# Optimization experiments

Hardware: AMD Instinct MI355X
Metric: run time of the kernel (lower is better)

The kernel has to match this reference:

```python
import math
import jax, jax.numpy as jnp
import numpy as np

NUM_HEADS = 16


def setup_inputs() -> dict:
    key = jax.random.key(0)
    ks = jax.random.split(key, 5)
    B, S, H = 2, 2048, 1024
    hidden_states = jax.random.normal(ks[0], (B, S, H), dtype=jnp.float32)
    # causal lower-triangular float mask [1, 1, S, S], as the module expects
    ltor_mask = jnp.tril(jnp.ones((S, S), dtype=jnp.float32))[None, None, :, :]
    # weights stored pre-transposed: y = x @ W + b (equivalent to torch Linear)
    W_qkv = jax.random.normal(ks[1], (H, 3 * H), dtype=jnp.float32) * (1.0 / math.sqrt(H))
    b_qkv = jnp.zeros((3 * H,), dtype=jnp.float32)
    W_dense = jax.random.normal(ks[2], (H, H), dtype=jnp.float32) * (1.0 / math.sqrt(H))
    b_dense = jnp.zeros((H,), dtype=jnp.float32)
    return {
        "hidden_states": hidden_states,
        "ltor_mask": ltor_mask,
        "W_qkv": W_qkv,
        "b_qkv": b_qkv,
        "W_dense": W_dense,
        "b_dense": b_dense,
    }


def reference(hidden_states, ltor_mask, W_qkv, b_qkv, W_dense, b_dense):
    B, S, H = hidden_states.shape
    nh = NUM_HEADS
    hd = H // nh

    # fused QKV projection: [B, S, 3H] -> split -> [B, nh, S, hd]
    qkv = hidden_states @ W_qkv + b_qkv
    q, k, v = jnp.split(qkv, 3, axis=-1)

    def to_heads(x):
        return x.reshape(B, S, nh, hd).transpose(0, 2, 1, 3)

    q, k, v = to_heads(q), to_heads(k), to_heads(v)

    # scaled dot-product scores [B, nh, S, S]
    scores = jnp.einsum("bhqd,bhkd->bhqk", q, k) / math.sqrt(hd)
    # mul/sub causal masking, exactly as the torch module does
    scores = scores * ltor_mask - 10000.0 * (1.0 - ltor_mask)
    probs = jax.nn.softmax(scores, axis=-1)
    # attention dropout omitted (eval mode / p=0.0)

    ctx = jnp.einsum("bhqk,bhkd->bhqd", probs, v)
    ctx = ctx.transpose(0, 2, 1, 3).reshape(B, S, H)

    out = ctx @ W_dense + b_dense
    # output dropout omitted (eval mode / p=0.0)
    return out
```

## Files before the change

kernel.cpp:

```cpp
#include <hip/hip_runtime.h>
#include <math.h>

#define BATCH 2
#define SEQ   2048
#define HID   1024
#define NHEAD 16
#define HDIM  64
#define MTOT  (BATCH * SEQ)
#define QKVN  (3 * HID)
#define HBUF  ((size_t)BATCH * NHEAD * SEQ * HDIM)

typedef _Float16 f16x8 __attribute__((ext_vector_type(8)));
typedef _Float16 f16x4 __attribute__((ext_vector_type(4)));
typedef float    f32x4 __attribute__((ext_vector_type(4)));

#define MFMA16(a, b, c) __builtin_amdgcn_mfma_f32_16x16x32_f16((a), (b), (c), 0, 0, 0)

#define GLDS16(gp, lp) __builtin_amdgcn_global_load_lds( \
    (const __attribute__((address_space(1))) void*)(gp), \
    (__attribute__((address_space(3))) void*)(lp), 16, 0, 0)

#if __has_builtin(__builtin_amdgcn_exp2f)
#define EXP2F(x) __builtin_amdgcn_exp2f(x)
#else
#define EXP2F(x) exp2f(x)
#endif

#define SCALE2 0.18033688011f
#define MASK2  -14426.950408f
#define BIAS2  -4.0f

__global__ __launch_bounds__(256) void prep_kernel(
    const float* __restrict__ hs, const float* __restrict__ Wqkv,
    const float* __restrict__ Wd, _Float16* __restrict__ A_h,
    _Float16* __restrict__ outQ, _Float16* __restrict__ outD)
{
    __shared__ _Float16 T[32][36];
    const int gid = blockIdx.x;
    const int tid = threadIdx.x;
    if (gid < 2048) {
        const int ci = gid * 256 + tid;
        const int m = ci >> 7, cc = ci & 127;
        const int g = cc >> 2, c = cc & 3;
        const float* src = hs + (size_t)m * 1024 + cc * 8;
        f16x8 o;
#pragma unroll
        for (int j = 0; j < 8; ++j) o[j] = (_Float16)src[j];
        *(f16x8*)(A_h + (size_t)m * 1024 + g * 32 + ((c ^ (m & 3)) << 3)) = o;
        return;
    }
    const int tb = gid - 2048;
    const int bx = tb & 127, k0 = (tb >> 7) * 32;
    const float* in;
    _Float16* out;
    int N, n0;
    if (bx < 96) { in = Wqkv; out = outQ; N = QKVN; n0 = bx * 32; }
    else         { in = Wd;   out = outD; N = HID;  n0 = (bx - 96) * 32; }
    {
        const int r = tid >> 3, c4 = (tid & 7) * 4;
        float4 v = *(const float4*)(in + (size_t)(k0 + r) * N + n0 + c4);
        T[r][c4 + 0] = (_Float16)v.x;
        T[r][c4 + 1] = (_Float16)v.y;
        T[r][c4 + 2] = (_Float16)v.z;
        T[r][c4 + 3] = (_Float16)v.w;
    }
    __syncthreads();
    {
        const int nn = tid >> 3, k4 = (tid & 7) * 4;
        const int n = n0 + nn;
        f16x4 o;
        o[0] = T[k4 + 0][nn]; o[1] = T[k4 + 1][nn];
        o[2] = T[k4 + 2][nn]; o[3] = T[k4 + 3][nn];
        const int pos = ((k4 >> 3) ^ (n & 3)), half = (k4 >> 2) & 1;
        *(f16x4*)(out + (size_t)n * 1024 + k0 + pos * 8 + half * 4) = o;
    }
}

__global__ __launch_bounds__(256) void transpose_v(
    const _Float16* __restrict__ v, _Float16* __restrict__ vt)
{
    __shared__ _Float16 T[64 * 64];
    const int s0 = blockIdx.x * 64;
    const size_t bh = (size_t)blockIdx.z * NHEAD + blockIdx.y;
    const int tid = threadIdx.x;
#pragma unroll
    for (int pass = 0; pass < 2; ++pass) {
        const int s = pass * 32 + (tid >> 3);
        const int c = tid & 7;
        f16x8 val = *(const f16x8*)(v + (bh * SEQ + s0 + s) * 64 + c * 8);
#pragma unroll
        for (int j = 0; j < 8; ++j) {
            const int d = c * 8 + j;
            T[d * 64 + (((s >> 3) ^ (d & 7)) << 3) + (s & 7)] = val[j];
        }
    }
    __syncthreads();
#pragma unroll
    for (int pass = 0; pass < 2; ++pass) {
        const int d = pass * 32 + (tid >> 3);
        const int cp = tid & 7;
        f16x8 val = *(const f16x8*)&T[d * 64 + cp * 8];
        *(f16x8*)(vt + (bh * 64 + d) * SEQ + s0 + cp * 8) = val;
    }
}

template<int EPI, int TM>
__global__ __launch_bounds__(256) void mfma_gemm(
    const _Float16* __restrict__ A, const _Float16* __restrict__ Bt,
    const float* __restrict__ bias, void* __restrict__ Cout,
    int M, int N, int K)
{
    __shared__ _Float16 As[TM * 32];
    __shared__ _Float16 Bs[128 * 32];
    constexpr int TI = TM / 32;
    constexpr int AR = TM / 4;

    const int tid = threadIdx.x;
    const int w = tid >> 6, l = tid & 63;
    const int a = l & 15, q4 = l >> 4;
    const int m0 = blockIdx.y * TM, n0 = blockIdx.x * 128;
    const int wm = (w >> 1) * (TM / 2), wn = (w & 1) * 64;

    f32x4 acc[TI][4];
#pragma unroll
    for (int i = 0; i < TI; ++i)
#pragma unroll
        for (int j = 0; j < 4; ++j) acc[i][j] = (f32x4){0.f, 0.f, 0.f, 0.f};

    const _Float16* gA = A + (size_t)(m0 + w * AR + (l >> 2)) * K + (l & 3) * 8;
    const _Float16* gB = Bt + (size_t)(n0 + w * 32 + (l >> 2)) * K + (l & 3) * 8;
    _Float16* sA = As + w * AR * 32;
    _Float16* sB = Bs + w * 1024;

    for (int k0 = 0; k0 < K; k0 += 32) {
#pragma unroll
        for (int u = 0; u < TM / 64; ++u)
            GLDS16(gA + (size_t)u * 16 * K + k0, sA + u * 512);
        GLDS16(gB + k0,          sB);
        GLDS16(gB + 16 * K + k0, sB + 512);
        __syncthreads();

        f16x8 af[TI], bf[4];
        const int pa = (q4 ^ (a & 3)) << 3;
#pragma unroll
        for (int i = 0; i < TI; ++i)
            af[i] = *(const f16x8*)&As[(wm + 16 * i + a) * 32 + pa];
#pragma unroll
        for (int j = 0; j < 4; ++j)
            bf[j] = *(const f16x8*)&Bs[(wn + 16 * j + a) * 32 + pa];
#pragma unroll
        for (int i = 0; i < TI; ++i)
#pragma unroll
            for (int j = 0; j < 4; ++j)
                acc[i][j] = MFMA16(af[i], bf[j], acc[i][j]);
        __syncthreads();
    }

    if (EPI == 0) {
        _Float16* base = (_Float16*)Cout;
#pragma unroll
        for (int j = 0; j < 4; ++j) {
            const int n = n0 + wn + 16 * j + a;
            const float bv = bias[n];
            const int t = n >> 10, h = (n >> 6) & 15, d = n & 63;
#pragma unroll
            for (int i = 0; i < TI; ++i) {
#pragma unroll
                for (int r = 0; r < 4; ++r) {
                    const int m = m0 + wm + 16 * i + q4 * 4 + r;
                    const int bb = m >> 11, s = m & 2047;
                    const _Float16 val = (_Float16)(acc[i][j][r] + bv);
                    if (t == 1) {
                        const int dk = ((((d >> 3) ^ (s & 7)) & 7) << 3) | (d & 7);
                        base[HBUF + ((size_t)(bb * 16 + h) * 2048 + s) * 64 + dk] = val;
                    } else {
                        base[(size_t)t * HBUF +
                             ((size_t)(bb * 16 + h) * 2048 + s) * 64 + d] = val;
                    }
                }
            }
        }
    } else {
        float* C = (float*)Cout;
#pragma unroll
        for (int j = 0; j < 4; ++j) {
            const int n = n0 + wn + 16 * j + a;
            const float bv = bias[n];
#pragma unroll
            for (int i = 0; i < TI; ++i)
#pragma unroll
                for (int r = 0; r < 4; ++r) {
                    const int m = m0 + wm + 16 * i + q4 * 4 + r;
                    C[(size_t)m * N + n] = acc[i][j][r] + bv;
                }
        }
    }
}

__global__ __launch_bounds__(256, 2) void attn_mfma(
    const _Float16* __restrict__ qb, const _Float16* __restrict__ kb,
    const _Float16* __restrict__ vtb, _Float16* __restrict__ ctx)
{
    __shared__ _Float16 Ks[2][64 * 64];
    __shared__ _Float16 VT[2][64 * 64];
    __shared__ _Float16 Ps[4][16 * 64];

    const int bid = blockIdx.x;
    const int jj = bid >> 3;
    const int bhIdx = (bid & 7) * 4 + (jj >> 4);
    const int p = jj & 15;
    const int b = bhIdx >> 4, h = bhIdx & 15;
    const int tid = threadIdx.x;
    const int w = tid >> 6, l = tid & 63;
    const int a = l & 15, q4 = l >> 4, a7 = a & 7;
    const size_t bh  = ((size_t)b * NHEAD + h) * SEQ;
    const size_t bhd = ((size_t)b * NHEAD + h) * 64;

    const int qHi = (31 - p) * 64 + w * 16;
    const int qLo = p * 64 + w * 16;
    const int ntiles = 32 - p;

    f16x8 qfh[2], qfl[2];
    {
        const _Float16* qp = qb + (bh + qHi + a) * 64;
        qfh[0] = *(const f16x8*)(qp + q4 * 8);
        qfh[1] = *(const f16x8*)(qp + 32 + q4 * 8);
        const _Float16* ql = qb + (bh + qLo + a) * 64;
        qfl[0] = *(const f16x8*)(ql + q4 * 8);
        qfl[1] = *(const f16x8*)(ql + 32 + q4 * 8);
    }

    f32x4 Oh[4], Ol[4];
#pragma unroll
    for (int c = 0; c < 4; ++c) {
        Oh[c] = (f32x4){0.f, 0.f, 0.f, 0.f};
        Ol[c] = (f32x4){0.f, 0.f, 0.f, 0.f};
    }
    float lh = 0.f, ll = 0.f;

    const _Float16* kg = kb + (bh + w * 16) * 64 + l * 8;
    const int vrow = w * 16 + (l >> 3);
    const _Float16* vg = vtb + (bhd + vrow) * 2048 + (l & 7) * 8;
    _Float16* pbuf = &Ps[w][0];
    const int p0 = (q4 ^ a7) << 3;

    auto stage = [&](int t, int buf) {
        _Float16* ksl = &Ks[buf][0] + w * 1024 + l * 8;
        const _Float16* kt = kg + (size_t)t * 4096;
        GLDS16(kt,       ksl);
        GLDS16(kt + 512, ksl + 512);
        _Float16* vtl = &VT[buf][0] + vrow * 64 + (l & 7) * 8;
        GLDS16(vg + t * 64,            vtl);
        GLDS16(vg + t * 64 + 8 * 2048, vtl + 512);
    };

    stage(0, 0);

    for (int t = 0; t < ntiles; ++t) {
        __syncthreads();
        if (t + 1 < ntiles) stage(t + 1, (t + 1) & 1);

        const _Float16* ksb  = &Ks[t & 1][0];
        const _Float16* vbuf = &VT[t & 1][0];
        const int kt0 = t * 64;
        const bool doLo = (t <= p);

        f32x4 sh[4], sl[4];
#pragma unroll
        for (int n0 = 0; n0 < 4; ++n0) {
            f16x8 kf0 = *(const f16x8*)&ksb[(n0 * 16 + a) * 64 + p0];
            f16x8 kf1 = *(const f16x8*)&ksb[(n0 * 16 + a) * 64 + (p0 ^ 32)];
            f32x4 c = (f32x4){0.f, 0.f, 0.f, 0.f};
            c = MFMA16(kf0, qfh[0], c);
            c = MFMA16(kf1, qfh[1], c);
            sh[n0] = c;
            if (doLo) {
                f32x4 d = (f32x4){0.f, 0.f, 0.f, 0.f};
                d = MFMA16(kf0, qfl[0], d);
                d = MFMA16(kf1, qfl[1], d);
                sl[n0] = d;
            }
        }

        auto half_step = [&](f32x4 st[4], float& lrun, f32x4* O,
                             const bool maskT, const int qbase) {
            if (maskT) {
#pragma unroll
                for (int n0 = 0; n0 < 4; ++n0)
#pragma unroll
                    for (int r = 0; r < 4; ++r) {
                        const int kgl = kt0 + n0 * 16 + q4 * 4 + r;
                        st[n0][r] = (kgl > qbase + a) ? MASK2
                                                      : fmaf(st[n0][r], SCALE2, BIAS2);
                    }
            } else {
#pragma unroll
                for (int n0 = 0; n0 < 4; ++n0)
#pragma unroll
                    for (int r = 0; r < 4; ++r)
                        st[n0][r] = fmaf(st[n0][r], SCALE2, BIAS2);
            }
            float ls = 0.f;
#pragma unroll
            for (int n0 = 0; n0 < 4; ++n0)
#pragma unroll
                for (int r = 0; r < 4; ++r) {
                    const float pe = EXP2F(st[n0][r]);
                    st[n0][r] = pe;
                    ls += pe;
                }
            lrun += ls;
#pragma unroll
            for (int n0 = 0; n0 < 4; ++n0) {
                f16x4 pk;
#pragma unroll
                for (int r = 0; r < 4; ++r) pk[r] = (_Float16)st[n0][r];
                const int pos = (2 * n0 + (q4 >> 1)) ^ a7;
                *(f16x4*)&pbuf[a * 64 + pos * 8 + ((q4 & 1) << 2)] = pk;
            }
            f16x8 pf0 = *(const f16x8*)&pbuf[a * 64 + p0];
            f16x8 pf1 = *(const f16x8*)&pbuf[a * 64 + (p0 ^ 32)];
#pragma unroll
            for (int c = 0; c < 4; ++c) {
                f16x8 vf0 = *(const f16x8*)&vbuf[(c * 16 + a) * 64 + p0];
                f16x8 vf1 = *(const f16x8*)&vbuf[(c * 16 + a) * 64 + (p0 ^ 32)];
                O[c] = MFMA16(vf0, pf0, O[c]);
                O[c] = MFMA16(vf1, pf1, O[c]);
            }
        };

        half_step(sh, lh, Oh, t == 31 - p, qHi);
        if (doLo) half_step(sl, ll, Ol, t == p, qLo);
    }

    auto finish = [&](float lrun, const f32x4* O, const int qbase) {
        float lt = lrun;
        lt += __shfl_xor(lt, 16);
        lt += __shfl_xor(lt, 32);
        const float inv = 1.0f / lt;
        const size_t row = (size_t)b * SEQ + qbase + a;
#pragma unroll
        for (int c = 0; c < 4; ++c) {
            const int d0 = c * 16 + q4 * 4;
            const int kcol = h * 64 + (d0 & ~31)
                           + ((((d0 >> 3) & 3) ^ (a & 3)) << 3) + (d0 & 7);
            f16x4 ov;
#pragma unroll
            for (int r = 0; r < 4; ++r) ov[r] = (_Float16)(O[c][r] * inv);
            *(f16x4*)(ctx + row * HID + kcol) = ov;
        }
    };
    finish(lh, Oh, qHi);
    finish(ll, Ol, qLo);
}

extern "C" void kernel_launch(void* const* d_in, const int* in_sizes, int n_in,
                              void* d_out, int out_size, void* d_ws, size_t ws_size,
                              hipStream_t stream) {
    const float* hs   = (const float*)d_in[0];
    const float* Wqkv = (const float*)d_in[2];
    const float* bqkv = (const float*)d_in[3];
    const float* Wd   = (const float*)d_in[4];
    const float* bd   = (const float*)d_in[5];

    _Float16* A_h   = (_Float16*)d_ws;
    _Float16* WqkvT = A_h + (size_t)MTOT * HID;
    _Float16* WdT   = WqkvT + (size_t)QKVN * HID;
    _Float16* qbuf  = WdT + (size_t)HID * HID;
    _Float16* ctxb  = qbuf + 4 * HBUF;

    prep_kernel<<<6144, 256, 0, stream>>>(hs, Wqkv, Wd, A_h, WqkvT, WdT);

    mfma_gemm<0, 128><<<dim3(QKVN / 128, MTOT / 128), 256, 0, stream>>>(
        A_h, WqkvT, bqkv, (void*)qbuf, MTOT, QKVN, HID);

    transpose_v<<<dim3(SEQ / 64, NHEAD, BATCH), 256, 0, stream>>>(
        qbuf + 2 * HBUF, qbuf + 3 * HBUF);

    attn_mfma<<<512, 256, 0, stream>>>(
        qbuf, qbuf + HBUF, qbuf + 3 * HBUF, ctxb);

    mfma_gemm<1, 64><<<dim3(HID / 128, MTOT / 64), 256, 0, stream>>>(
        ctxb, WdT, bd, d_out, MTOT, HID, HID);
}
```

Measured before the change: 196.9 us.

## Fuse V transpose into QKV GEMM epilogue and stage stores through LDS

Drops the separate transpose_v kernel by having the QKV GEMM epilogue write V directly in transposed [d][s] layout, staging each warp's output tile in shared memory so global writes become 16-byte vector stores. Q and K tiles (with K's swizzle) and the dense GEMM's fp32 output are also staged through LDS for coalesced vector stores instead of scattered scalar writes. Shared memory grows to a single 36 KB buffer reused for the epilogue, which may reduce occupancy.

```diff
diff --git a/kernel.cpp b/kernel.cpp
--- a/kernel.cpp
+++ b/kernel.cpp
@@ -76,42 +76,15 @@
     }
 }
 
-__global__ __launch_bounds__(256) void transpose_v(
-    const _Float16* __restrict__ v, _Float16* __restrict__ vt)
-{
-    __shared__ _Float16 T[64 * 64];
-    const int s0 = blockIdx.x * 64;
-    const size_t bh = (size_t)blockIdx.z * NHEAD + blockIdx.y;
-    const int tid = threadIdx.x;
-#pragma unroll
-    for (int pass = 0; pass < 2; ++pass) {
-        const int s = pass * 32 + (tid >> 3);
-        const int c = tid & 7;
-        f16x8 val = *(const f16x8*)(v + (bh * SEQ + s0 + s) * 64 + c * 8);
-#pragma unroll
-        for (int j = 0; j < 8; ++j) {
-            const int d = c * 8 + j;
-            T[d * 64 + (((s >> 3) ^ (d & 7)) << 3) + (s & 7)] = val[j];
-        }
-    }
-    __syncthreads();
-#pragma unroll
-    for (int pass = 0; pass < 2; ++pass) {
-        const int d = pass * 32 + (tid >> 3);
-        const int cp = tid & 7;
-        f16x8 val = *(const f16x8*)&T[d * 64 + cp * 8];
-        *(f16x8*)(vt + (bh * 64 + d) * SEQ + s0 + cp * 8) = val;
-    }
-}
-
 template<int EPI, int TM>
 __global__ __launch_bounds__(256) void mfma_gemm(
     const _Float16* __restrict__ A, const _Float16* __restrict__ Bt,
     const float* __restrict__ bias, void* __restrict__ Cout,
     int M, int N, int K)
 {
-    __shared__ _Float16 As[TM * 32];
-    __shared__ _Float16 Bs[128 * 32];
+    __shared__ __align__(16) char SMEM[36864];
+    _Float16* As = (_Float16*)SMEM;
+    _Float16* Bs = As + TM * 32;
     constexpr int TI = TM / 32;
     constexpr int AR = TM / 4;
 
@@ -157,42 +130,76 @@
     }
 
     if (EPI == 0) {
+        const int nbase = n0 + wn;
+        const int t = nbase >> 10, h = (nbase >> 6) & 15;
+        const int bb = (m0 + wm) >> 11;
+        const int sbase = (m0 + wm) & 2047;
         _Float16* base = (_Float16*)Cout;
-#pragma unroll
-        for (int j = 0; j < 4; ++j) {
-            const int n = n0 + wn + 16 * j + a;
-            const float bv = bias[n];
-            const int t = n >> 10, h = (n >> 6) & 15, d = n & 63;
-#pragma unroll
-            for (int i = 0; i < TI; ++i) {
-#pragma unroll
-                for (int r = 0; r < 4; ++r) {
-                    const int m = m0 + wm + 16 * i + q4 * 4 + r;
-                    const int bb = m >> 11, s = m & 2047;
-                    const _Float16 val = (_Float16)(acc[i][j][r] + bv);
-                    if (t == 1) {
-                        const int dk = ((((d >> 3) ^ (s & 7)) & 7) << 3) | (d & 7);
-                        base[HBUF + ((size_t)(bb * 16 + h) * 2048 + s) * 64 + dk] = val;
-                    } else {
-                        base[(size_t)t * HBUF +
-                             ((size_t)(bb * 16 + h) * 2048 + s) * 64 + d] = val;
-                    }
+        _Float16* Cw = (_Float16*)SMEM + w * 4608;
+        const int lsub = l >> 3, c = l & 7;
+        if (t != 2) {
+#pragma unroll
+            for (int j = 0; j < 4; ++j) {
+                const float bv = bias[nbase + 16 * j + a];
+#pragma unroll
+                for (int i = 0; i < 4; ++i)
+#pragma unroll
+                    for (int r = 0; r < 4; ++r)
+                        Cw[(16 * i + q4 * 4 + r) * 72 + 16 * j + a] =
+                            (_Float16)(acc[i][j][r] + bv);
+            }
+            const int cswz = (t == 1) ? (c ^ lsub) : c;
+            _Float16* gq = base + (size_t)t * HBUF
+                         + ((size_t)(bb * 16 + h) * 2048 + sbase) * 64;
+#pragma unroll
+            for (int pp = 0; pp < 8; ++pp) {
+                const int lr = pp * 8 + lsub;
+                f16x8 v8 = *(const f16x8*)&Cw[lr * 72 + cswz * 8];
+                *(f16x8*)(gq + (size_t)lr * 64 + c * 8) = v8;
+            }
+        } else {
+#pragma unroll
+            for (int j = 0; j < 4; ++j) {
+                const float bv = bias[nbase + 16 * j + a];
+#pragma unroll
+                for (int i = 0; i < 4; ++i) {
+                    f16x4 pk;
+#pragma unroll
+                    for (int r = 0; r < 4; ++r)
+                        pk[r] = (_Float16)(acc[i][j][r] + bv);
+                    *(f16x4*)&Cw[(16 * j + a) * 72 + 16 * i + q4 * 4] = pk;
                 }
+            }
+            const int cswz = c ^ lsub;
+            _Float16* gv = base + 2 * HBUF
+                         + ((size_t)(bb * 16 + h) * 64) * 2048 + sbase;
+#pragma unroll
+            for (int pp = 0; pp < 8; ++pp) {
+                const int d = pp * 8 + lsub;
+                f16x8 v8 = *(const f16x8*)&Cw[d * 72 + cswz * 8];
+                *(f16x8*)(gv + (size_t)d * 2048 + c * 8) = v8;
             }
         }
     } else {
         float* C = (float*)Cout;
+        float* Cw = (float*)SMEM + w * 2176;
 #pragma unroll
         for (int j = 0; j < 4; ++j) {
-            const int n = n0 + wn + 16 * j + a;
-            const float bv = bias[n];
+            const float bv = bias[n0 + wn + 16 * j + a];
 #pragma unroll
             for (int i = 0; i < TI; ++i)
 #pragma unroll
-                for (int r = 0; r < 4; ++r) {
-                    const int m = m0 + wm + 16 * i + q4 * 4 + r;
-                    C[(size_t)m * N + n] = acc[i][j][r] + bv;
-                }
+                for (int r = 0; r < 4; ++r)
+                    Cw[(16 * i + q4 * 4 + r) * 68 + 16 * j + a] =
+                        acc[i][j][r] + bv;
+        }
+        const int lsub = l >> 4, c = l & 15;
+        float* gout = C + (size_t)(m0 + wm) * N + n0 + wn;
+#pragma unroll
+        for (int pp = 0; pp < 8; ++pp) {
+            const int lr = pp * 4 + lsub;
+            float4 v4 = *(const float4*)&Cw[lr * 68 + c * 4];
+            *(float4*)(gout + (size_t)lr * N + c * 4) = v4;
         }
     }
 }
@@ -367,18 +374,15 @@
     _Float16* WqkvT = A_h + (size_t)MTOT * HID;
     _Float16* WdT   = WqkvT + (size_t)QKVN * HID;
     _Float16* qbuf  = WdT + (size_t)HID * HID;
-    _Float16* ctxb  = qbuf + 4 * HBUF;
+    _Float16* ctxb  = qbuf + 3 * HBUF;
 
     prep_kernel<<<6144, 256, 0, stream>>>(hs, Wqkv, Wd, A_h, WqkvT, WdT);
 
     mfma_gemm<0, 128><<<dim3(QKVN / 128, MTOT / 128), 256, 0, stream>>>(
         A_h, WqkvT, bqkv, (void*)qbuf, MTOT, QKVN, HID);
 
-    transpose_v<<<dim3(SEQ / 64, NHEAD, BATCH), 256, 0, stream>>>(
-        qbuf + 2 * HBUF, qbuf + 3 * HBUF);
-
     attn_mfma<<<512, 256, 0, stream>>>(
-        qbuf, qbuf + HBUF, qbuf + 3 * HBUF, ctxb);
+        qbuf, qbuf + HBUF, qbuf + 2 * HBUF, ctxb);
 
     mfma_gemm<1, 64><<<dim3(HID / 128, MTOT / 64), 256, 0, stream>>>(
         ctxb, WdT, bd, d_out, MTOT, HID, HID);
```

Measured after the change: 205.0 us. +4.1%, slower.
